# Performance work log

Measured on AMD Instinct MI355X. Metric: run time of the kernel, lower is better.

## Reference

```python
import jax, jax.numpy as jnp
import numpy as np

WINDOW = (2, 7, 7)
NUM_HEADS = 8


def _relative_position_index(ws):
    d, h, w = ws
    coords = np.stack(np.meshgrid(np.arange(d), np.arange(h), np.arange(w), indexing='ij'), 0)
    cf = coords.reshape(3, -1)                      # [3, N]
    rel = (cf[:, :, None] - cf[:, None, :]).transpose(1, 2, 0)  # [N, N, 3]
    rel[..., 0] += d - 1
    rel[..., 1] += h - 1
    rel[..., 2] += w - 1
    idx = rel[..., 0] * ((2 * h - 1) * (2 * w - 1)) + rel[..., 1] * (2 * w - 1) + rel[..., 2]
    return idx.astype(np.int32)                     # [N, N]

_REL_IDX = _relative_position_index(WINDOW)


def setup_inputs() -> dict:
    key = jax.random.key(0)
    ks = jax.random.split(key, 6)
    B_, N, C = 2048, 98, 256
    nW = 64
    table_size = (2 * WINDOW[0] - 1) * (2 * WINDOW[1] - 1) * (2 * WINDOW[2] - 1)  # 507
    return {
        'x': jax.random.normal(ks[0], (B_, N, C), jnp.float32),
        'mask': jax.random.normal(ks[1], (nW, N, N), jnp.float32),
        'qkv_w': jax.random.normal(ks[2], (C, 3 * C), jnp.float32) * 0.02,
        'proj_w': jax.random.normal(ks[3], (C, C), jnp.float32) * 0.02,
        'proj_b': jax.random.normal(ks[4], (C,), jnp.float32) * 0.02,
        'bias_table': jax.random.normal(ks[5], (table_size, NUM_HEADS), jnp.float32) * 0.02,
    }


def reference(x, mask, qkv_w, proj_w, proj_b, bias_table):
    B_, N, C = x.shape
    H = NUM_HEADS
    Dh = C // H
    scale = Dh ** (-0.5)

    qkv = jnp.einsum('bnc,cd->bnd', x, qkv_w)               # [B_, N, 3C]
    qkv = qkv.reshape(B_, N, 3, H, Dh).transpose(2, 0, 3, 1, 4)  # [3, B_, H, N, Dh]
    q, k, v = qkv[0], qkv[1], qkv[2]

    attn = jnp.einsum('bhnd,bhmd->bhnm', q * scale, k)      # [B_, H, N, N]

    rel_idx = jnp.asarray(_REL_IDX[:N, :N])
    bias = bias_table[rel_idx.reshape(-1)].reshape(N, N, H).transpose(2, 0, 1)  # [H, N, N]
    attn = attn + bias[None]

    nW = mask.shape[0]
    attn = attn.reshape(B_ // nW, nW, H, N, N) + mask[None, :, None, :, :]
    attn = attn.reshape(B_, H, N, N)
    attn = jax.nn.softmax(attn, axis=-1)

    out = jnp.einsum('bhnm,bhmd->bhnd', attn, v)            # [B_, H, N, Dh]
    out = out.transpose(0, 2, 1, 3).reshape(B_, N, C)
    out = jnp.einsum('bnc,cd->bnd', out, proj_w) + proj_b
    return out
```

## Files before the change

### kernel.cpp

```cpp
#include <hip/hip_runtime.h>
#include <stdint.h>

typedef __bf16 bf16_t;
typedef __bf16 bf16x8 __attribute__((ext_vector_type(8)));
typedef float f32x4 __attribute__((ext_vector_type(4)));

#define MFMA16(a, b, c) __builtin_amdgcn_mfma_f32_16x16x32_bf16(a, b, c, 0, 0, 0)

__device__ __forceinline__ void gload_lds16(const bf16_t* g, bf16_t* l) {
  __builtin_amdgcn_global_load_lds(
      (const __attribute__((address_space(1))) void*)g,
      (__attribute__((address_space(3))) void*)l, 16, 0, 0);
}

__device__ __forceinline__ int sw4(int i) {
  return ((i & 3) << 2) | ((i >> 2) & 3);
}

__global__ __launch_bounds__(256) void cvt_x_k(const float* __restrict__ x,
                                               bf16_t* __restrict__ xb, int n8) {
  int i = blockIdx.x * 256 + threadIdx.x;
  if (i >= n8) return;
  const float4* xp = (const float4*)x + (size_t)i * 2;
  float4 f0 = xp[0], f1 = xp[1];
  bf16x8 o = {(bf16_t)f0.x, (bf16_t)f0.y, (bf16_t)f0.z, (bf16_t)f0.w,
              (bf16_t)f1.x, (bf16_t)f1.y, (bf16_t)f1.z, (bf16_t)f1.w};
  *(bf16x8*)(xb + (size_t)i * 8) = o;
}

__global__ __launch_bounds__(256) void cvt_wT_k(const float* __restrict__ w,
                                                bf16_t* __restrict__ wT, int N) {
  int n = blockIdx.x, k = threadIdx.x;
  wT[(size_t)n * 256 + k] = (bf16_t)w[(size_t)k * N + n];
}

__global__ __launch_bounds__(256) void gemm256(const bf16_t* __restrict__ A,
                                               const bf16_t* __restrict__ BT,
                                               int ncols,
                                               bf16_t* __restrict__ outb,
                                               float* __restrict__ outf,
                                               const float* __restrict__ bias) {
  __shared__ __align__(16) bf16_t sA[128 * 64];
  __shared__ __align__(16) bf16_t sB[128 * 64];
  const int tid = threadIdx.x;
  const int lane = tid & 63, wave = tid >> 6;
  const int lm = lane & 15, quad = lane >> 4;

  int nwg = gridDim.x * gridDim.y;
  int L = blockIdx.y * gridDim.x + blockIdx.x;
  if ((nwg & 7) == 0) {
    int cpx = nwg >> 3;
    L = (L & 7) * cpx + (L >> 3);
  }
  const int bx = L % gridDim.x, by = L / gridDim.x;

  const int mBase = by * 128;
  const int nBase = bx * 128;
  const int wm = (wave >> 1) * 64, wn = (wave & 1) * 64;

  f32x4 acc[4][4];
#pragma unroll
  for (int i = 0; i < 4; i++)
#pragma unroll
    for (int j = 0; j < 4; j++) acc[i][j] = {0.f, 0.f, 0.f, 0.f};

  const bf16_t* Ab = A + (size_t)mBase * 256;
  const bf16_t* Bb = BT + (size_t)nBase * 256;

  for (int kb = 0; kb < 4; ++kb) {
    const int k0 = kb * 64;
#pragma unroll
    for (int it = 0; it < 4; ++it) {
      int cid = it * 256 + wave * 64 + lane;
      int row = cid >> 3, kcp = cid & 7;
      int kcl = kcp ^ (row & 7);
      bf16_t* dstA = sA + (it * 256 + wave * 64) * 8;
      bf16_t* dstB = sB + (it * 256 + wave * 64) * 8;
      gload_lds16(Ab + (size_t)row * 256 + k0 + kcl * 8, dstA);
      gload_lds16(Bb + (size_t)row * 256 + k0 + kcl * 8, dstB);
    }
    __syncthreads();
#pragma unroll
    for (int kk = 0; kk < 64; kk += 32) {
      int c = (kk >> 3) + quad;
      bf16x8 af[4], bfr[4];
#pragma unroll
      for (int mt = 0; mt < 4; mt++) {
        int m = wm + mt * 16 + lm;
        af[mt] = *(const bf16x8*)(sA + m * 64 + ((c ^ (m & 7)) << 3));
      }
#pragma unroll
      for (int nt = 0; nt < 4; nt++) {
        int n = wn + nt * 16 + lm;
        bfr[nt] = *(const bf16x8*)(sB + n * 64 + ((c ^ (n & 7)) << 3));
      }
#pragma unroll
      for (int mt = 0; mt < 4; mt++)
#pragma unroll
        for (int nt = 0; nt < 4; nt++)
          acc[mt][nt] = MFMA16(af[mt], bfr[nt], acc[mt][nt]);
    }
    __syncthreads();
  }

  if (outb) {
#pragma unroll
    for (int mt = 0; mt < 4; mt++)
#pragma unroll
      for (int nt = 0; nt < 4; nt++) {
        int col = nBase + wn + nt * 16 + lm;
        int rbase = mBase + wm + mt * 16 + quad * 4;
#pragma unroll
        for (int r = 0; r < 4; r++)
          outb[(size_t)(rbase + r) * ncols + col] = (bf16_t)acc[mt][nt][r];
      }
  } else {
#pragma unroll
    for (int mt = 0; mt < 4; mt++)
#pragma unroll
      for (int nt = 0; nt < 4; nt++) {
        int col = nBase + wn + nt * 16 + lm;
        float bv = bias[col];
        int rbase = mBase + wm + mt * 16 + quad * 4;
#pragma unroll
        for (int r = 0; r < 4; r++)
          outf[(size_t)(rbase + r) * ncols + col] = acc[mt][nt][r] + bv;
      }
  }
}

__global__ __launch_bounds__(512, 4) void attn_win(
    const bf16_t* __restrict__ qkv, const float* __restrict__ mask,
    const float* __restrict__ btab, bf16_t* __restrict__ y) {
  __shared__ __align__(16) bf16_t sP[2][112 * 128];
  __shared__ __align__(16) bf16_t sVT[2][32 * 128];
  __shared__ float sTab[2][512];
  __shared__ int sU[112];

  const int tid = threadIdx.x;
  const int p = blockIdx.x, b = blockIdx.y;
  const int lane = tid & 63, wave = tid >> 6;
  const int w4 = wave & 3, hg = wave >> 2;
  const int h = 2 * p + hg;
  const int lm = lane & 15, quad = lane >> 4;

  {
    uint4 z = {0, 0, 0, 0};
    uint4* pp = (uint4*)&sP[0][0];
    for (int i = tid; i < 2 * 112 * 128 / 8; i += 512) pp[i] = z;
  }
  for (int idx = tid; idx < 2048; idx += 512) {
    int g = idx >> 10, r = idx & 1023;
    int d = r >> 5, j = 96 + (r & 31);
    if (j >= 98)
      sVT[g][d * 128 + (((j >> 3) ^ sw4(d & 15)) << 3) + (j & 7)] = (bf16_t)0.f;
  }
  for (int idx = tid; idx < 1024; idx += 512) {
    int g = idx >> 9, i = idx & 511;
    if (i < 507) sTab[g][i] = btab[i * 8 + 2 * p + g];
  }
  if (tid < 112) {
    int n = tid;
    int d = n / 49, r = n - d * 49;
    int hh = r / 7, w = r - hh * 7;
    sU[tid] = (n < 98) ? (d * 169 + hh * 13 + w) : 0;
  }

  const bf16_t* qh = qkv + (size_t)b * 98 * 768 + h * 32;

  {
    int j = tid & 127, q2 = (tid >> 7) & 1, g = tid >> 8;
    const bf16_t* qv = qkv + (size_t)b * 98 * 768 + (2 * p + g) * 32;
    if (j < 98) {
#pragma unroll
      for (int t = 0; t < 2; t++) {
        int dc = q2 + 2 * t;
        bf16x8 v8 = *(const bf16x8*)(qv + (size_t)j * 768 + 512 + dc * 8);
#pragma unroll
        for (int e = 0; e < 8; e++) {
          int d = dc * 8 + e;
          sVT[g][d * 128 + (((j >> 3) ^ sw4(d & 15)) << 3) + (j & 7)] = v8[e];
        }
      }
    }
  }
  __syncthreads();

  bf16x8 kf[7];
#pragma unroll
  for (int ct = 0; ct < 7; ct++)
    kf[ct] =
        *(const bf16x8*)(qh + (size_t)(ct * 16 + lm) * 768 + 256 + quad * 8);

  f32x4 s4[2][7];
#pragma unroll
  for (int rti = 0; rti < 2; rti++) {
    int rt = w4 + rti * 4;
    if (rt <= 6) {
      bf16x8 qf = *(const bf16x8*)(qh + (size_t)(rt * 16 + lm) * 768 + quad * 8);
#pragma unroll
      for (int ct = 0; ct < 7; ct++) {
        f32x4 z = {0.f, 0.f, 0.f, 0.f};
        s4[rti][ct] = MFMA16(qf, kf[ct], z);
      }
    }
  }

  const float* mp = mask + (size_t)(b & 63) * 9604;
  const float scale = 0.17677669529663687f;
  float inv[2][4];

#pragma unroll
  for (int rti = 0; rti < 2; rti++) {
    int rt = w4 + rti * 4;
    if (rt > 6) continue;
    int ib = rt * 16 + quad * 4;
    int ui[4], rb[4];
#pragma unroll
    for (int r = 0; r < 4; r++) {
      int i = ib + r;
      ui[r] = sU[i] + 253;
      rb[r] = (i < 98 ? i : 97) * 98;
    }
#pragma unroll
    for (int ct = 0; ct < 7; ct++) {
      int j = ct * 16 + lm;
      int uj = sU[j];
      int jc = j < 98 ? j : 97;
      bool jv = j < 98;
#pragma unroll
      for (int r = 0; r < 4; r++) {
        float v = s4[rti][ct][r] * scale + sTab[hg][ui[r] - uj] + mp[rb[r] + jc];
        s4[rti][ct][r] = jv ? v : -1e30f;
      }
    }
#pragma unroll
    for (int r = 0; r < 4; r++) {
      float mx = s4[rti][0][r];
#pragma unroll
      for (int ct = 1; ct < 7; ct++) mx = fmaxf(mx, s4[rti][ct][r]);
#pragma unroll
      for (int o = 1; o < 16; o <<= 1) mx = fmaxf(mx, __shfl_xor(mx, o));
      float sum = 0.f;
#pragma unroll
      for (int ct = 0; ct < 7; ct++) {
        float e = __expf(s4[rti][ct][r] - mx);
        s4[rti][ct][r] = e;
        sum += e;
      }
#pragma unroll
      for (int o = 1; o < 16; o <<= 1) sum += __shfl_xor(sum, o);
      inv[rti][r] = 1.f / sum;
    }
#pragma unroll
    for (int ct = 0; ct < 7; ct++) {
      int c2 = 2 * ct + (lm >> 3);
      int j7 = lm & 7;
#pragma unroll
      for (int r = 0; r < 4; r++) {
        int i = ib + r;
        sP[hg][i * 128 + ((c2 ^ (4 * r + quad)) << 3) + j7] =
            (bf16_t)s4[rti][ct][r];
      }
    }
  }
  __syncthreads();

  bf16x8 vf[2][4];
#pragma unroll
  for (int dt = 0; dt < 2; dt++)
#pragma unroll
    for (int kk = 0; kk < 4; kk++) {
      int d = dt * 16 + lm;
      vf[dt][kk] = *(const bf16x8*)(sVT[hg] + d * 128 +
                                    (((4 * kk + quad) ^ sw4(lm)) << 3));
    }
  bf16_t* yb = y + (size_t)b * 98 * 256 + h * 32;
#pragma unroll
  for (int rti = 0; rti < 2; rti++) {
    int rt = w4 + rti * 4;
    if (rt > 6) continue;
    bf16x8 af[4];
#pragma unroll
    for (int kk = 0; kk < 4; kk++) {
      int i = rt * 16 + lm;
      af[kk] = *(const bf16x8*)(sP[hg] + i * 128 +
                                (((4 * kk + quad) ^ sw4(lm)) << 3));
    }
#pragma unroll
    for (int dt = 0; dt < 2; dt++) {
      f32x4 o = {0.f, 0.f, 0.f, 0.f};
#pragma unroll
      for (int kk = 0; kk < 4; kk++) o = MFMA16(af[kk], vf[dt][kk], o);
#pragma unroll
      for (int r = 0; r < 4; r++) {
        int i = rt * 16 + quad * 4 + r;
        if (i < 98)
          yb[(size_t)i * 256 + dt * 16 + lm] = (bf16_t)(o[r] * inv[rti][r]);
      }
    }
  }
}

extern "C" void kernel_launch(void* const* d_in, const int* in_sizes, int n_in,
                              void* d_out, int out_size, void* d_ws,
                              size_t ws_size, hipStream_t stream) {
  const float* x = (const float*)d_in[0];
  const float* mask = (const float*)d_in[1];
  const float* qkv_w = (const float*)d_in[2];
  const float* proj_w = (const float*)d_in[3];
  const float* proj_b = (const float*)d_in[4];
  const float* btab = (const float*)d_in[5];
  float* out = (float*)d_out;

  char* ws = (char*)d_ws;
  bf16_t* qkv = (bf16_t*)ws;
  bf16_t* ybuf = (bf16_t*)(ws + 308281344);
  bf16_t* xb = ybuf;
  bf16_t* wT = (bf16_t*)(ws + 308281344 + 102760448);
  bf16_t* pT = (bf16_t*)(ws + 308281344 + 102760448 + 393216);

  cvt_x_k<<<25088, 256, 0, stream>>>(x, xb, 6422528);
  cvt_wT_k<<<768, 256, 0, stream>>>(qkv_w, wT, 768);
  cvt_wT_k<<<256, 256, 0, stream>>>(proj_w, pT, 256);

  gemm256<<<dim3(6, 1568), 256, 0, stream>>>(xb, wT, 768, qkv, nullptr,
                                             nullptr);

  attn_win<<<dim3(4, 2048), 512, 0, stream>>>(qkv, mask, btab, ybuf);

  gemm256<<<dim3(2, 1568), 256, 0, stream>>>(ybuf, pT, 256, nullptr, out,
                                             proj_b);
}
```

Measured before the change: 863.1 us.

## Make attention blocks persistent over 8 windows with prefetch of next Q/K/V

The attention kernel now launches 256 instead of 2048 window-blocks per head pair, and each block loops over 8 windows with a stride of 256. Setup of the bias table, index map and zeroed padding is done once per block rather than per window. Q/K/V fragments for the next window are loaded into registers while the current window's softmax and PV run. The two weight-transpose kernels are merged into one launch. The risks are higher register pressure and fewer blocks to spread across CUs.

```diff
diff --git a/kernel.cpp b/kernel.cpp
--- a/kernel.cpp
+++ b/kernel.cpp
@@ -28,10 +28,17 @@
   *(bf16x8*)(xb + (size_t)i * 8) = o;
 }
 
-__global__ __launch_bounds__(256) void cvt_wT_k(const float* __restrict__ w,
-                                                bf16_t* __restrict__ wT, int N) {
-  int n = blockIdx.x, k = threadIdx.x;
-  wT[(size_t)n * 256 + k] = (bf16_t)w[(size_t)k * N + n];
+__global__ __launch_bounds__(256) void cvt_w2_k(const float* __restrict__ w1,
+                                                bf16_t* __restrict__ o1,
+                                                const float* __restrict__ w2,
+                                                bf16_t* __restrict__ o2) {
+  int blk = blockIdx.x, k = threadIdx.x;
+  if (blk < 768) {
+    o1[(size_t)blk * 256 + k] = (bf16_t)w1[(size_t)k * 768 + blk];
+  } else {
+    int n = blk - 768;
+    o2[(size_t)n * 256 + k] = (bf16_t)w2[(size_t)k * 256 + n];
+  }
 }
 
 __global__ __launch_bounds__(256) void gemm256(const bf16_t* __restrict__ A,
@@ -138,11 +145,12 @@
   __shared__ int sU[112];
 
   const int tid = threadIdx.x;
-  const int p = blockIdx.x, b = blockIdx.y;
+  const int p = blockIdx.x, by = blockIdx.y;
   const int lane = tid & 63, wave = tid >> 6;
   const int w4 = wave & 3, hg = wave >> 2;
   const int h = 2 * p + hg;
   const int lm = lane & 15, quad = lane >> 4;
+  const int sj = tid & 127, sq2 = (tid >> 7) & 1, sg = tid >> 8;
 
   {
     uint4 z = {0, 0, 0, 0};
@@ -156,8 +164,8 @@
       sVT[g][d * 128 + (((j >> 3) ^ sw4(d & 15)) << 3) + (j & 7)] = (bf16_t)0.f;
   }
   for (int idx = tid; idx < 1024; idx += 512) {
-    int g = idx >> 9, i = idx & 511;
-    if (i < 507) sTab[g][i] = btab[i * 8 + 2 * p + g];
+    int g = idx >> 9, i2 = idx & 511;
+    if (i2 < 507) sTab[g][i2] = btab[i2 * 8 + 2 * p + g];
   }
   if (tid < 112) {
     int n = tid;
@@ -166,139 +174,197 @@
     sU[tid] = (n < 98) ? (d * 169 + hh * 13 + w) : 0;
   }
 
-  const bf16_t* qh = qkv + (size_t)b * 98 * 768 + h * 32;
-
-  {
-    int j = tid & 127, q2 = (tid >> 7) & 1, g = tid >> 8;
-    const bf16_t* qv = qkv + (size_t)b * 98 * 768 + (2 * p + g) * 32;
-    if (j < 98) {
-#pragma unroll
-      for (int t = 0; t < 2; t++) {
-        int dc = q2 + 2 * t;
-        bf16x8 v8 = *(const bf16x8*)(qv + (size_t)j * 768 + 512 + dc * 8);
-#pragma unroll
-        for (int e = 0; e < 8; e++) {
-          int d = dc * 8 + e;
-          sVT[g][d * 128 + (((j >> 3) ^ sw4(d & 15)) << 3) + (j & 7)] = v8[e];
-        }
-      }
-    }
-  }
-  __syncthreads();
-
-  bf16x8 kf[7];
+  const size_t bstr = 98 * 768;
+  const bf16_t* qh = qkv + (size_t)by * bstr + h * 32;
+  const bf16_t* qv = qkv + (size_t)by * bstr + (2 * p + sg) * 32;
+
+  bf16x8 kf[7], qf[2], vv[2];
 #pragma unroll
   for (int ct = 0; ct < 7; ct++)
     kf[ct] =
         *(const bf16x8*)(qh + (size_t)(ct * 16 + lm) * 768 + 256 + quad * 8);
-
-  f32x4 s4[2][7];
+  qf[0] = *(const bf16x8*)(qh + (size_t)(w4 * 16 + lm) * 768 + quad * 8);
+  if (w4 < 3)
+    qf[1] =
+        *(const bf16x8*)(qh + (size_t)((w4 + 4) * 16 + lm) * 768 + quad * 8);
+  if (sj < 98) {
+    vv[0] = *(const bf16x8*)(qv + (size_t)sj * 768 + 512 + sq2 * 8);
+    vv[1] = *(const bf16x8*)(qv + (size_t)sj * 768 + 512 + (sq2 + 2) * 8);
+  }
+
+  __syncthreads();
+
+  const float* mp = mask + (size_t)(by & 63) * 9604;
+  const float scale = 0.17677669529663687f;
+  int uj7[7];
+#pragma unroll
+  for (int ct = 0; ct < 7; ct++) uj7[ct] = sU[ct * 16 + lm];
+  int ui_[2][4], rbo[2][4];
 #pragma unroll
   for (int rti = 0; rti < 2; rti++) {
+    if (rti == 1 && w4 == 3) continue;
     int rt = w4 + rti * 4;
-    if (rt <= 6) {
-      bf16x8 qf = *(const bf16x8*)(qh + (size_t)(rt * 16 + lm) * 768 + quad * 8);
+    int ib = rt * 16 + quad * 4;
+#pragma unroll
+    for (int r = 0; r < 4; r++) {
+      int i = ib + r;
+      ui_[rti][r] = sU[i] + 253;
+      rbo[rti][r] = (i < 98 ? i : 97) * 98;
+    }
+  }
+
+  int bcur = by;
+  for (int it2 = 0; it2 < 8; ++it2) {
+    const bool more = (it2 < 7);
+    const bf16_t* qhn = qh + 256 * bstr;
+    const bf16_t* qvn = qv + 256 * bstr;
+
+#pragma unroll
+    for (int rti = 0; rti < 2; rti++) {
+      if (rti == 1 && w4 == 3) continue;
+#pragma unroll
+      for (int r = 0; r < 4; r++) {
+        asm volatile("" : "+v"(ui_[rti][r]));
+        asm volatile("" : "+v"(rbo[rti][r]));
+      }
+    }
+
+    if (sj < 98) {
+#pragma unroll
+      for (int t = 0; t < 2; t++) {
+        int dc = sq2 + 2 * t;
+#pragma unroll
+        for (int e = 0; e < 8; e++) {
+          int d = dc * 8 + e;
+          sVT[sg][d * 128 + (((sj >> 3) ^ sw4(d & 15)) << 3) + (sj & 7)] =
+              vv[t][e];
+        }
+      }
+    }
+    __syncthreads();
+
+    f32x4 s4[2][7];
+#pragma unroll
+    for (int rti = 0; rti < 2; rti++) {
+      if (rti == 1 && w4 == 3) continue;
 #pragma unroll
       for (int ct = 0; ct < 7; ct++) {
         f32x4 z = {0.f, 0.f, 0.f, 0.f};
-        s4[rti][ct] = MFMA16(qf, kf[ct], z);
-      }
-    }
-  }
-
-  const float* mp = mask + (size_t)(b & 63) * 9604;
-  const float scale = 0.17677669529663687f;
-  float inv[2][4];
-
-#pragma unroll
-  for (int rti = 0; rti < 2; rti++) {
-    int rt = w4 + rti * 4;
-    if (rt > 6) continue;
-    int ib = rt * 16 + quad * 4;
-    int ui[4], rb[4];
-#pragma unroll
-    for (int r = 0; r < 4; r++) {
-      int i = ib + r;
-      ui[r] = sU[i] + 253;
-      rb[r] = (i < 98 ? i : 97) * 98;
-    }
-#pragma unroll
-    for (int ct = 0; ct < 7; ct++) {
-      int j = ct * 16 + lm;
-      int uj = sU[j];
-      int jc = j < 98 ? j : 97;
-      bool jv = j < 98;
+        s4[rti][ct] = MFMA16(qf[rti], kf[ct], z);
+      }
+    }
+
+    if (more) {
+      if (sj < 98) {
+        vv[0] = *(const bf16x8*)(qvn + (size_t)sj * 768 + 512 + sq2 * 8);
+        vv[1] = *(const bf16x8*)(qvn + (size_t)sj * 768 + 512 + (sq2 + 2) * 8);
+      }
+      qf[0] = *(const bf16x8*)(qhn + (size_t)(w4 * 16 + lm) * 768 + quad * 8);
+      if (w4 < 3)
+        qf[1] = *(const bf16x8*)(qhn + (size_t)((w4 + 4) * 16 + lm) * 768 +
+                                 quad * 8);
+    }
+
+    float inv[2][4];
+#pragma unroll
+    for (int rti = 0; rti < 2; rti++) {
+      if (rti == 1 && w4 == 3) continue;
+#pragma unroll
+      for (int ct = 0; ct < 7; ct++) {
+        int j = ct * 16 + lm;
+        int jc = j < 98 ? j : 97;
+        bool jv = j < 98;
+#pragma unroll
+        for (int r = 0; r < 4; r++) {
+          float v = s4[rti][ct][r] * scale +
+                    sTab[hg][ui_[rti][r] - uj7[ct]] + mp[rbo[rti][r] + jc];
+          s4[rti][ct][r] = jv ? v : -1e30f;
+        }
+      }
 #pragma unroll
       for (int r = 0; r < 4; r++) {
-        float v = s4[rti][ct][r] * scale + sTab[hg][ui[r] - uj] + mp[rb[r] + jc];
-        s4[rti][ct][r] = jv ? v : -1e30f;
-      }
-    }
-#pragma unroll
-    for (int r = 0; r < 4; r++) {
-      float mx = s4[rti][0][r];
-#pragma unroll
-      for (int ct = 1; ct < 7; ct++) mx = fmaxf(mx, s4[rti][ct][r]);
-#pragma unroll
-      for (int o = 1; o < 16; o <<= 1) mx = fmaxf(mx, __shfl_xor(mx, o));
-      float sum = 0.f;
+        float mx = s4[rti][0][r];
+#pragma unroll
+        for (int ct = 1; ct < 7; ct++) mx = fmaxf(mx, s4[rti][ct][r]);
+#pragma unroll
+        for (int o = 1; o < 16; o <<= 1) mx = fmaxf(mx, __shfl_xor(mx, o));
+        float sum = 0.f;
+#pragma unroll
+        for (int ct = 0; ct < 7; ct++) {
+          float e = __expf(s4[rti][ct][r] - mx);
+          s4[rti][ct][r] = e;
+          sum += e;
+        }
+#pragma unroll
+        for (int o = 1; o < 16; o <<= 1) sum += __shfl_xor(sum, o);
+        inv[rti][r] = 1.f / sum;
+      }
+    }
+
+    if (more) {
+#pragma unroll
+      for (int ct = 0; ct < 7; ct++)
+        kf[ct] = *(const bf16x8*)(qhn + (size_t)(ct * 16 + lm) * 768 + 256 +
+                                  quad * 8);
+    }
+
+#pragma unroll
+    for (int rti = 0; rti < 2; rti++) {
+      if (rti == 1 && w4 == 3) continue;
+      int rt = w4 + rti * 4;
+      int ib = rt * 16 + quad * 4;
 #pragma unroll
       for (int ct = 0; ct < 7; ct++) {
-        float e = __expf(s4[rti][ct][r] - mx);
-        s4[rti][ct][r] = e;
-        sum += e;
-      }
-#pragma unroll
-      for (int o = 1; o < 16; o <<= 1) sum += __shfl_xor(sum, o);
-      inv[rti][r] = 1.f / sum;
-    }
-#pragma unroll
-    for (int ct = 0; ct < 7; ct++) {
-      int c2 = 2 * ct + (lm >> 3);
-      int j7 = lm & 7;
-#pragma unroll
-      for (int r = 0; r < 4; r++) {
-        int i = ib + r;
-        sP[hg][i * 128 + ((c2 ^ (4 * r + quad)) << 3) + j7] =
-            (bf16_t)s4[rti][ct][r];
-      }
-    }
-  }
-  __syncthreads();
-
-  bf16x8 vf[2][4];
-#pragma unroll
-  for (int dt = 0; dt < 2; dt++)
-#pragma unroll
-    for (int kk = 0; kk < 4; kk++) {
-      int d = dt * 16 + lm;
-      vf[dt][kk] = *(const bf16x8*)(sVT[hg] + d * 128 +
-                                    (((4 * kk + quad) ^ sw4(lm)) << 3));
-    }
-  bf16_t* yb = y + (size_t)b * 98 * 256 + h * 32;
-#pragma unroll
-  for (int rti = 0; rti < 2; rti++) {
-    int rt = w4 + rti * 4;
-    if (rt > 6) continue;
-    bf16x8 af[4];
-#pragma unroll
-    for (int kk = 0; kk < 4; kk++) {
-      int i = rt * 16 + lm;
-      af[kk] = *(const bf16x8*)(sP[hg] + i * 128 +
-                                (((4 * kk + quad) ^ sw4(lm)) << 3));
-    }
-#pragma unroll
-    for (int dt = 0; dt < 2; dt++) {
-      f32x4 o = {0.f, 0.f, 0.f, 0.f};
-#pragma unroll
-      for (int kk = 0; kk < 4; kk++) o = MFMA16(af[kk], vf[dt][kk], o);
-#pragma unroll
-      for (int r = 0; r < 4; r++) {
-        int i = rt * 16 + quad * 4 + r;
-        if (i < 98)
-          yb[(size_t)i * 256 + dt * 16 + lm] = (bf16_t)(o[r] * inv[rti][r]);
-      }
-    }
+        int c2 = 2 * ct + (lm >> 3);
+        int j7 = lm & 7;
+#pragma unroll
+        for (int r = 0; r < 4; r++) {
+          int i = ib + r;
+          sP[hg][i * 128 + ((c2 ^ (4 * r + quad)) << 3) + j7] =
+              (bf16_t)s4[rti][ct][r];
+        }
+      }
+    }
+
+    bf16x8 vf2[2][4];
+#pragma unroll
+    for (int dt = 0; dt < 2; dt++)
+#pragma unroll
+      for (int kk = 0; kk < 4; kk++) {
+        int d = dt * 16 + lm;
+        vf2[dt][kk] = *(const bf16x8*)(sVT[hg] + d * 128 +
+                                       (((4 * kk + quad) ^ sw4(lm)) << 3));
+      }
+    bf16_t* yb = y + (size_t)bcur * 98 * 256 + h * 32;
+#pragma unroll
+    for (int rti = 0; rti < 2; rti++) {
+      if (rti == 1 && w4 == 3) continue;
+      int rt = w4 + rti * 4;
+      bf16x8 af[4];
+#pragma unroll
+      for (int kk = 0; kk < 4; kk++) {
+        int i = rt * 16 + lm;
+        af[kk] = *(const bf16x8*)(sP[hg] + i * 128 +
+                                  (((4 * kk + quad) ^ sw4(lm)) << 3));
+      }
+#pragma unroll
+      for (int dt = 0; dt < 2; dt++) {
+        f32x4 o = {0.f, 0.f, 0.f, 0.f};
+#pragma unroll
+        for (int kk = 0; kk < 4; kk++) o = MFMA16(af[kk], vf2[dt][kk], o);
+#pragma unroll
+        for (int r = 0; r < 4; r++) {
+          int i = rt * 16 + quad * 4 + r;
+          if (i < 98)
+            yb[(size_t)i * 256 + dt * 16 + lm] = (bf16_t)(o[r] * inv[rti][r]);
+        }
+      }
+    }
+    __syncthreads();
+
+    qh = qhn;
+    qv = qvn;
+    bcur += 256;
   }
 }
 
@@ -321,13 +387,12 @@
   bf16_t* pT = (bf16_t*)(ws + 308281344 + 102760448 + 393216);
 
   cvt_x_k<<<25088, 256, 0, stream>>>(x, xb, 6422528);
-  cvt_wT_k<<<768, 256, 0, stream>>>(qkv_w, wT, 768);
-  cvt_wT_k<<<256, 256, 0, stream>>>(proj_w, pT, 256);
+  cvt_w2_k<<<1024, 256, 0, stream>>>(qkv_w, wT, proj_w, pT);
 
   gemm256<<<dim3(6, 1568), 256, 0, stream>>>(xb, wT, 768, qkv, nullptr,
                                              nullptr);
 
-  attn_win<<<dim3(4, 2048), 512, 0, stream>>>(qkv, mask, btab, ybuf);
+  attn_win<<<dim3(4, 256), 512, 0, stream>>>(qkv, mask, btab, ybuf);
 
   gemm256<<<dim3(2, 1568), 256, 0, stream>>>(ybuf, pT, 256, nullptr, out,
                                              proj_b);
```

Result: slower. 1.611 ms (+86.6%).
